# Performance work log

Measured on AMD Instinct MI355X. Metric: run time of the kernel, lower is better.

Reference implementation:

```python
import jax, jax.numpy as jnp
import numpy as np

B, S, D, A = 64, 2048, 512, 512


def setup_inputs() -> dict:
    key = jax.random.key(0)
    ks = jax.random.split(key, 6)
    return {
        "input": jax.random.normal(ks[0], (B, D), dtype=jnp.float32),
        "context": jax.random.normal(ks[1], (B, S, D), dtype=jnp.float32),
        "Wh": jax.random.uniform(ks[2], (D, A), dtype=jnp.float32, minval=-0.1, maxval=0.1),
        "Ws": jax.random.uniform(ks[3], (D, A), dtype=jnp.float32, minval=-0.1, maxval=0.1),
        "b_attn": jax.random.uniform(ks[4], (A,), dtype=jnp.float32, minval=-0.1, maxval=0.1),
        "va": jax.random.uniform(ks[5], (A,), dtype=jnp.float32, minval=-0.1, maxval=0.1),
    }


def reference(input, context, Wh, Ws, b_attn, va):
    # _concat score: tanh(ht@Wh + context@Ws + b) @ va  -> [B, S]
    ht_proj = input @ Wh                      # [B, A]
    ctx_proj = jnp.einsum("bsd,da->bsa", context, Ws)  # [B, S, A]
    concat = jnp.tanh(ht_proj[:, None, :] + ctx_proj + b_attn)  # [B, S, A]
    attn = jnp.einsum("bsa,a->bs", concat, va)  # [B, S]
    # padding mask: positions whose mean feature is exactly 0
    context_mask = jnp.mean(context, axis=-1) == 0  # [B, S]
    attn = jnp.where(context_mask, -jnp.inf, attn)
    attn_dist = jax.nn.softmax(attn, axis=1)  # [B, S]
    attn_context = jnp.einsum("bsd,bs->bd", context, attn_dist)  # [B, D]
    return attn_context, attn_dist
```

## Files before the change

### kernel.cpp

```cpp
#include <hip/hip_runtime.h>
#include <hip/hip_bf16.h>
#include <math.h>

#define B_ 64
#define S_ 2048
#define D_ 512
#define A_ 512

typedef __attribute__((ext_vector_type(8))) short short8;
typedef __attribute__((ext_vector_type(4))) short short4b;
typedef __attribute__((ext_vector_type(4))) float f32x4;

__device__ __forceinline__ short bf16b(float f) {
    __hip_bfloat16 h = __float2bfloat16(f);
    union { __hip_bfloat16 h; short s; } u; u.h = h;
    return u.s;
}

__device__ __forceinline__ float tanh_fast(float x) {
    float e = __expf(2.0f * x);
    return 1.0f - 2.0f / (e + 1.0f);
}

__device__ __forceinline__ void llds16(const void* g, void* l) {
    __builtin_amdgcn_global_load_lds(
        (const __attribute__((address_space(1))) unsigned int*)g,
        (__attribute__((address_space(3))) unsigned int*)l, 16, 0, 0);
}

__global__ __launch_bounds__(256) void k_htw(const float* __restrict__ input,
                                             const float* __restrict__ Wh,
                                             const float* __restrict__ b_attn,
                                             float* __restrict__ htWb) {
    __shared__ float xin[512];
    const int b = blockIdx.x, t = threadIdx.x;
    xin[t] = input[b * D_ + t];
    xin[t + 256] = input[b * D_ + t + 256];
    __syncthreads();
    float a0 = 0.f, a1 = 0.f;
#pragma unroll 8
    for (int d = 0; d < D_; ++d) {
        const float xv = xin[d];
        a0 += xv * Wh[d * A_ + t];
        a1 += xv * Wh[d * A_ + t + 256];
    }
    htWb[b * A_ + t] = a0 + b_attn[t];
    htWb[b * A_ + t + 256] = a1 + b_attn[t + 256];
}

__global__ __launch_bounds__(256) void k_wst(const float* __restrict__ Ws,
                                             short* __restrict__ WsT) {
    const int bx = blockIdx.x & 7, by = blockIdx.x >> 3;
    const int r0 = by * 64, c0 = bx * 64;
    __shared__ short tile[64][72];
    const int t = threadIdx.x;
    const int row = t >> 4, col4 = (t & 15) * 4;
#pragma unroll
    for (int i = 0; i < 4; ++i) {
        const float4 v = *(const float4*)&Ws[(r0 + row + i * 16) * A_ + c0 + col4];
        tile[col4 + 0][row + i * 16] = bf16b(v.x);
        tile[col4 + 1][row + i * 16] = bf16b(v.y);
        tile[col4 + 2][row + i * 16] = bf16b(v.z);
        tile[col4 + 3][row + i * 16] = bf16b(v.w);
    }
    __syncthreads();
#pragma unroll
    for (int i = 0; i < 4; ++i) {
        const int arow = row + i * 16;
        short4b o;
        o.x = tile[arow][col4 + 0];
        o.y = tile[arow][col4 + 1];
        o.z = tile[arow][col4 + 2];
        o.w = tile[arow][col4 + 3];
        *(short4b*)&WsT[(c0 + arow) * D_ + r0 + col4] = o;
    }
}

__global__ __launch_bounds__(512, 4)
void k_score(const float* __restrict__ ctx, const short* __restrict__ WsT,
             const float* __restrict__ htWb, const float* __restrict__ va,
             float* __restrict__ scores) {
    __shared__ __align__(16) short Ab[2][64 * 32];
    __shared__ __align__(16) short Bb[2][512 * 32];
    __shared__ float hv_s[512];
    __shared__ float va_s[512];
    __shared__ float scores_s[64];
    __shared__ float rowsum_s[64];

    const int tid = threadIdx.x;
    const int w = tid >> 6, lane = tid & 63;
    const int wm = w >> 2, wn = w & 3;
    const int tile = blockIdx.x;
    const int b = tile >> 5;
    const int s0 = (tile & 31) * 64;
    const long rowbase = (long)b * S_ + s0;

    hv_s[tid] = htWb[b * A_ + tid];
    va_s[tid] = va[tid];
    if (tid < 64) scores_s[tid] = 0.f;

    const int arow = tid >> 3, kq = tid & 7;
    const float* aSrc = ctx + (rowbase + arow) * D_ + kq * 4;
    float rowsum_acc = 0.f;

    f32x4 acc[2][8];
#pragma unroll
    for (int i = 0; i < 2; ++i)
#pragma unroll
        for (int j = 0; j < 8; ++j)
#pragma unroll
            for (int e = 0; e < 4; ++e) acc[i][j][e] = 0.f;

#define STAGE_B(buf, kt)                                                      \
    {                                                                         \
        _Pragma("unroll") for (int j = 0; j < 4; ++j) {                       \
            const int a = (w * 4 + j) * 16 + (lane >> 2);                     \
            const int c = lane & 3;                                           \
            const int csw = c ^ ((a >> 1) & 3);                               \
            llds16(WsT + a * D_ + (kt) * 32 + csw * 8,                        \
                   (void*)&Bb[buf][(w * 4 + j) * 512]);                       \
        }                                                                     \
    }

#define STAGE_A_WRITE(buf, v)                                                 \
    {                                                                         \
        rowsum_acc += (v).x + (v).y + (v).z + (v).w;                          \
        short4b o;                                                            \
        o.x = bf16b((v).x); o.y = bf16b((v).y);                               \
        o.z = bf16b((v).z); o.w = bf16b((v).w);                               \
        const int cw = kq >> 1, sub = kq & 1;                                 \
        const int csw = cw ^ ((arow >> 1) & 3);                               \
        *(short4b*)((char*)&Ab[buf][0] + arow * 64 + csw * 16 + sub * 8) = o; \
    }

    STAGE_B(0, 0);
    {
        const float4 v = *(const float4*)(aSrc);
        STAGE_A_WRITE(0, v);
    }
    __syncthreads();

    for (int kt = 0; kt < 16; ++kt) {
        const int cur = kt & 1;
        float4 nv;
        if (kt < 15) {
            nv = *(const float4*)(aSrc + (kt + 1) * 32);
            STAGE_B(cur ^ 1, kt + 1);
        }
        {
            short8 af[2];
#pragma unroll
            for (int mf = 0; mf < 2; ++mf) {
                const int r = wm * 32 + mf * 16 + (lane & 15);
                const int c = lane >> 4;
                const int csw = c ^ ((r >> 1) & 3);
                af[mf] = *(const short8*)((const char*)&Ab[cur][0] + r * 64 + csw * 16);
            }
#pragma unroll
            for (int nf = 0; nf < 8; ++nf) {
                const int a = wn * 128 + nf * 16 + (lane & 15);
                const int c = lane >> 4;
                const int csw = c ^ ((a >> 1) & 3);
                const short8 bf =
                    *(const short8*)((const char*)&Bb[cur][0] + a * 64 + csw * 16);
                acc[0][nf] = __builtin_amdgcn_mfma_f32_16x16x32_bf16(af[0], bf, acc[0][nf], 0, 0, 0);
                acc[1][nf] = __builtin_amdgcn_mfma_f32_16x16x32_bf16(af[1], bf, acc[1][nf], 0, 0, 0);
            }
        }
        if (kt < 15) STAGE_A_WRITE(cur ^ 1, nv);
        __syncthreads();
    }

    rowsum_acc += __shfl_xor(rowsum_acc, 1);
    rowsum_acc += __shfl_xor(rowsum_acc, 2);
    rowsum_acc += __shfl_xor(rowsum_acc, 4);
    if ((tid & 7) == 0) rowsum_s[arow] = rowsum_acc;

    float hv[8], vv[8];
#pragma unroll
    for (int nf = 0; nf < 8; ++nf) {
        const int col = wn * 128 + nf * 16 + (lane & 15);
        hv[nf] = hv_s[col];
        vv[nf] = va_s[col];
    }
#pragma unroll
    for (int mf = 0; mf < 2; ++mf) {
#pragma unroll
        for (int r = 0; r < 4; ++r) {
            float p = 0.f;
#pragma unroll
            for (int nf = 0; nf < 8; ++nf)
                p += vv[nf] * tanh_fast(hv[nf] + acc[mf][nf][r]);
            p += __shfl_xor(p, 1);
            p += __shfl_xor(p, 2);
            p += __shfl_xor(p, 4);
            p += __shfl_xor(p, 8);
            if ((lane & 15) == 0) {
                const int row = wm * 32 + mf * 16 + (lane >> 4) * 4 + r;
                atomicAdd(&scores_s[row], p);
            }
        }
    }
    __syncthreads();

    if (tid < 64) {
        float sc = scores_s[tid];
        if (rowsum_s[tid] == 0.0f) sc = -__builtin_inff();
        scores[rowbase + tid] = sc;
    }
}

__global__ __launch_bounds__(256) void k_softmax(float* __restrict__ dist) {
    const int b = blockIdx.x, t = threadIdx.x;
    float* p = dist + b * S_;
    float v[8];
    float m = -__builtin_inff();
#pragma unroll
    for (int i = 0; i < 8; ++i) {
        v[i] = p[t + i * 256];
        m = fmaxf(m, v[i]);
    }
#pragma unroll
    for (int mask = 1; mask < 64; mask <<= 1) m = fmaxf(m, __shfl_xor(m, mask));
    __shared__ float redm[4], reds[4];
    if ((t & 63) == 0) redm[t >> 6] = m;
    __syncthreads();
    m = fmaxf(fmaxf(redm[0], redm[1]), fmaxf(redm[2], redm[3]));
    float sum = 0.f;
#pragma unroll
    for (int i = 0; i < 8; ++i) {
        v[i] = __expf(v[i] - m);
        sum += v[i];
    }
#pragma unroll
    for (int mask = 1; mask < 64; mask <<= 1) sum += __shfl_xor(sum, mask);
    if ((t & 63) == 0) reds[t >> 6] = sum;
    __syncthreads();
    sum = reds[0] + reds[1] + reds[2] + reds[3];
    const float inv = 1.0f / sum;
#pragma unroll
    for (int i = 0; i < 8; ++i) p[t + i * 256] = v[i] * inv;
}

__global__ __launch_bounds__(256) void k_wsum(const float* __restrict__ ctx,
                                              const float* __restrict__ dist,
                                              float* __restrict__ partial) {
    const int ch = blockIdx.x, b = blockIdx.y;
    const int t = threadIdx.x;
    __shared__ float ps[128];
    if (t < 128) ps[t] = dist[b * S_ + ch * 128 + t];
    __syncthreads();
    const float* cbase = ctx + ((long)b * S_ + ch * 128) * D_;
    float ax = 0.f, ay = 0.f;
#pragma unroll 4
    for (int r = 0; r < 128; ++r) {
        const float2 cv = *(const float2*)&cbase[r * D_ + t * 2];
        ax += ps[r] * cv.x;
        ay += ps[r] * cv.y;
    }
    float2 o; o.x = ax; o.y = ay;
    *(float2*)&partial[((b * 16 + ch) * D_) + t * 2] = o;
}

__global__ __launch_bounds__(256) void k_reduce(const float* __restrict__ partial,
                                                float* __restrict__ out) {
    const int b = blockIdx.x, t = threadIdx.x;
    float ax = 0.f, ay = 0.f;
#pragma unroll
    for (int j = 0; j < 16; ++j) {
        const float2 v = *(const float2*)&partial[((b * 16 + j) * D_) + t * 2];
        ax += v.x;
        ay += v.y;
    }
    float2 o; o.x = ax; o.y = ay;
    *(float2*)&out[b * D_ + t * 2] = o;
}

extern "C" void kernel_launch(void* const* d_in, const int* in_sizes, int n_in,
                              void* d_out, int out_size, void* d_ws, size_t ws_size,
                              hipStream_t stream) {
    (void)in_sizes; (void)n_in; (void)out_size; (void)ws_size;
    const float* input  = (const float*)d_in[0];
    const float* ctx    = (const float*)d_in[1];
    const float* Wh     = (const float*)d_in[2];
    const float* Ws     = (const float*)d_in[3];
    const float* b_attn = (const float*)d_in[4];
    const float* va     = (const float*)d_in[5];

    float* out = (float*)d_out;
    float* attn_ctx  = out;
    float* attn_dist = out + B_ * D_;

    char* ws = (char*)d_ws;
    float* htWb    = (float*)ws;
    short* WsT     = (short*)(ws + 131072);
    float* partial = (float*)(ws + 131072 + 524288);

    k_htw<<<64, 256, 0, stream>>>(input, Wh, b_attn, htWb);
    k_wst<<<64, 256, 0, stream>>>(Ws, WsT);
    k_score<<<2048, 512, 0, stream>>>(ctx, WsT, htWb, va, attn_dist);
    k_softmax<<<64, 256, 0, stream>>>(attn_dist);
    k_wsum<<<dim3(16, 64), 256, 0, stream>>>(ctx, attn_dist, partial);
    k_reduce<<<64, 256, 0, stream>>>(partial, attn_ctx);
}
```

Before: 507.6 us.

## Double score-kernel M tile to 128 rows and widen wsum loads to float4

```diff
diff --git a/kernel.cpp b/kernel.cpp
--- a/kernel.cpp
+++ b/kernel.cpp
@@ -76,36 +76,36 @@
     }
 }
 
-__global__ __launch_bounds__(512, 4)
-void k_score(const float* __restrict__ ctx, const short* __restrict__ WsT,
-             const float* __restrict__ htWb, const float* __restrict__ va,
-             float* __restrict__ scores) {
-    __shared__ __align__(16) short Ab[2][64 * 32];
+__global__ __launch_bounds__(512, 2)
+void k_score2(const float* __restrict__ ctx, const short* __restrict__ WsT,
+              const float* __restrict__ htWb, const float* __restrict__ va,
+              float* __restrict__ scores) {
+    __shared__ __align__(16) short Ab[2][128 * 32];
     __shared__ __align__(16) short Bb[2][512 * 32];
     __shared__ float hv_s[512];
     __shared__ float va_s[512];
-    __shared__ float scores_s[64];
-    __shared__ float rowsum_s[64];
+    __shared__ float scores_s[128];
+    __shared__ float rowsum_s[128];
 
     const int tid = threadIdx.x;
     const int w = tid >> 6, lane = tid & 63;
     const int wm = w >> 2, wn = w & 3;
-    const int tile = blockIdx.x;
-    const int b = tile >> 5;
-    const int s0 = (tile & 31) * 64;
+    const int blk = blockIdx.x;
+    const int b = blk >> 4;
+    const int s0 = (blk & 15) * 128;
     const long rowbase = (long)b * S_ + s0;
 
     hv_s[tid] = htWb[b * A_ + tid];
     va_s[tid] = va[tid];
-    if (tid < 64) scores_s[tid] = 0.f;
-
-    const int arow = tid >> 3, kq = tid & 7;
-    const float* aSrc = ctx + (rowbase + arow) * D_ + kq * 4;
+    if (tid < 128) scores_s[tid] = 0.f;
+
+    const int arow = tid >> 2, aq = tid & 2 * 2 - 1;
+    const float* aSrc = ctx + (rowbase + arow) * (long)D_;
     float rowsum_acc = 0.f;
 
-    f32x4 acc[2][8];
-#pragma unroll
-    for (int i = 0; i < 2; ++i)
+    f32x4 acc[4][8];
+#pragma unroll
+    for (int i = 0; i < 4; ++i)
 #pragma unroll
         for (int j = 0; j < 8; ++j)
 #pragma unroll
@@ -122,36 +122,42 @@
         }                                                                     \
     }
 
-#define STAGE_A_WRITE(buf, v)                                                 \
+#define STAGE_A_WRITE(buf, v0, v1)                                            \
     {                                                                         \
-        rowsum_acc += (v).x + (v).y + (v).z + (v).w;                          \
-        short4b o;                                                            \
-        o.x = bf16b((v).x); o.y = bf16b((v).y);                               \
-        o.z = bf16b((v).z); o.w = bf16b((v).w);                               \
-        const int cw = kq >> 1, sub = kq & 1;                                 \
-        const int csw = cw ^ ((arow >> 1) & 3);                               \
-        *(short4b*)((char*)&Ab[buf][0] + arow * 64 + csw * 16 + sub * 8) = o; \
+        rowsum_acc += (v0).x + (v0).y + (v0).z + (v0).w;                      \
+        rowsum_acc += (v1).x + (v1).y + (v1).z + (v1).w;                      \
+        short4b o0, o1;                                                       \
+        o0.x = bf16b((v0).x); o0.y = bf16b((v0).y);                           \
+        o0.z = bf16b((v0).z); o0.w = bf16b((v0).w);                           \
+        o1.x = bf16b((v1).x); o1.y = bf16b((v1).y);                           \
+        o1.z = bf16b((v1).z); o1.w = bf16b((v1).w);                           \
+        const int sw = (arow >> 1) & 3;                                       \
+        const int c0 = (aq >> 1), c1 = 2 + (aq >> 1), sub = aq & 1;           \
+        *(short4b*)((char*)&Ab[buf][0] + arow * 64 + ((c0 ^ sw) * 16) + sub * 8) = o0; \
+        *(short4b*)((char*)&Ab[buf][0] + arow * 64 + ((c1 ^ sw) * 16) + sub * 8) = o1; \
     }
 
     STAGE_B(0, 0);
     {
-        const float4 v = *(const float4*)(aSrc);
-        STAGE_A_WRITE(0, v);
+        const float4 v0 = *(const float4*)(aSrc + aq * 4);
+        const float4 v1 = *(const float4*)(aSrc + aq * 4 + 16);
+        STAGE_A_WRITE(0, v0, v1);
     }
     __syncthreads();
 
     for (int kt = 0; kt < 16; ++kt) {
         const int cur = kt & 1;
-        float4 nv;
+        float4 nv0, nv1;
         if (kt < 15) {
-            nv = *(const float4*)(aSrc + (kt + 1) * 32);
             STAGE_B(cur ^ 1, kt + 1);
+            nv0 = *(const float4*)(aSrc + (kt + 1) * 32 + aq * 4);
+            nv1 = *(const float4*)(aSrc + (kt + 1) * 32 + aq * 4 + 16);
         }
         {
-            short8 af[2];
-#pragma unroll
-            for (int mf = 0; mf < 2; ++mf) {
-                const int r = wm * 32 + mf * 16 + (lane & 15);
+            short8 af[4];
+#pragma unroll
+            for (int mf = 0; mf < 4; ++mf) {
+                const int r = wm * 64 + mf * 16 + (lane & 15);
                 const int c = lane >> 4;
                 const int csw = c ^ ((r >> 1) & 3);
                 af[mf] = *(const short8*)((const char*)&Ab[cur][0] + r * 64 + csw * 16);
@@ -163,18 +169,19 @@
                 const int csw = c ^ ((a >> 1) & 3);
                 const short8 bf =
                     *(const short8*)((const char*)&Bb[cur][0] + a * 64 + csw * 16);
-                acc[0][nf] = __builtin_amdgcn_mfma_f32_16x16x32_bf16(af[0], bf, acc[0][nf], 0, 0, 0);
-                acc[1][nf] = __builtin_amdgcn_mfma_f32_16x16x32_bf16(af[1], bf, acc[1][nf], 0, 0, 0);
+#pragma unroll
+                for (int mf = 0; mf < 4; ++mf)
+                    acc[mf][nf] = __builtin_amdgcn_mfma_f32_16x16x32_bf16(
+                        af[mf], bf, acc[mf][nf], 0, 0, 0);
             }
         }
-        if (kt < 15) STAGE_A_WRITE(cur ^ 1, nv);
+        if (kt < 15) STAGE_A_WRITE(cur ^ 1, nv0, nv1);
         __syncthreads();
     }
 
     rowsum_acc += __shfl_xor(rowsum_acc, 1);
     rowsum_acc += __shfl_xor(rowsum_acc, 2);
-    rowsum_acc += __shfl_xor(rowsum_acc, 4);
-    if ((tid & 7) == 0) rowsum_s[arow] = rowsum_acc;
+    if ((tid & 3) == 0) rowsum_s[arow] = rowsum_acc;
 
     float hv[8], vv[8];
 #pragma unroll
@@ -184,26 +191,26 @@
         vv[nf] = va_s[col];
     }
 #pragma unroll
-    for (int mf = 0; mf < 2; ++mf) {
-#pragma unroll
-        for (int r = 0; r < 4; ++r) {
+    for (int mf = 0; mf < 4; ++mf) {
+#pragma unroll
+        for (int e = 0; e < 4; ++e) {
             float p = 0.f;
 #pragma unroll
             for (int nf = 0; nf < 8; ++nf)
-                p += vv[nf] * tanh_fast(hv[nf] + acc[mf][nf][r]);
+                p += vv[nf] * tanh_fast(hv[nf] + acc[mf][nf][e]);
             p += __shfl_xor(p, 1);
             p += __shfl_xor(p, 2);
             p += __shfl_xor(p, 4);
             p += __shfl_xor(p, 8);
             if ((lane & 15) == 0) {
-                const int row = wm * 32 + mf * 16 + (lane >> 4) * 4 + r;
+                const int row = wm * 64 + mf * 16 + (lane >> 4) * 4 + e;
                 atomicAdd(&scores_s[row], p);
             }
         }
     }
     __syncthreads();
 
-    if (tid < 64) {
+    if (tid < 128) {
         float sc = scores_s[tid];
         if (rowsum_s[tid] == 0.0f) sc = -__builtin_inff();
         scores[rowbase + tid] = sc;
@@ -242,38 +249,40 @@
     for (int i = 0; i < 8; ++i) p[t + i * 256] = v[i] * inv;
 }
 
-__global__ __launch_bounds__(256) void k_wsum(const float* __restrict__ ctx,
+__global__ __launch_bounds__(128) void k_wsum(const float* __restrict__ ctx,
                                               const float* __restrict__ dist,
                                               float* __restrict__ partial) {
     const int ch = blockIdx.x, b = blockIdx.y;
     const int t = threadIdx.x;
     __shared__ float ps[128];
-    if (t < 128) ps[t] = dist[b * S_ + ch * 128 + t];
+    ps[t] = dist[b * S_ + ch * 128 + t];
     __syncthreads();
     const float* cbase = ctx + ((long)b * S_ + ch * 128) * D_;
-    float ax = 0.f, ay = 0.f;
+    float ax = 0.f, ay = 0.f, az = 0.f, aw = 0.f;
 #pragma unroll 4
     for (int r = 0; r < 128; ++r) {
-        const float2 cv = *(const float2*)&cbase[r * D_ + t * 2];
-        ax += ps[r] * cv.x;
-        ay += ps[r] * cv.y;
-    }
-    float2 o; o.x = ax; o.y = ay;
-    *(float2*)&partial[((b * 16 + ch) * D_) + t * 2] = o;
-}
-
-__global__ __launch_bounds__(256) void k_reduce(const float* __restrict__ partial,
+        const float4 cv = *(const float4*)&cbase[r * D_ + t * 4];
+        const float pw = ps[r];
+        ax += pw * cv.x;
+        ay += pw * cv.y;
+        az += pw * cv.z;
+        aw += pw * cv.w;
+    }
+    float4 o; o.x = ax; o.y = ay; o.z = az; o.w = aw;
+    *(float4*)&partial[((b * 16 + ch) * D_) + t * 4] = o;
+}
+
+__global__ __launch_bounds__(128) void k_reduce(const float* __restrict__ partial,
                                                 float* __restrict__ out) {
     const int b = blockIdx.x, t = threadIdx.x;
-    float ax = 0.f, ay = 0.f;
+    float ax = 0.f, ay = 0.f, az = 0.f, aw = 0.f;
 #pragma unroll
     for (int j = 0; j < 16; ++j) {
-        const float2 v = *(const float2*)&partial[((b * 16 + j) * D_) + t * 2];
-        ax += v.x;
-        ay += v.y;
-    }
-    float2 o; o.x = ax; o.y = ay;
-    *(float2*)&out[b * D_ + t * 2] = o;
+        const float4 v = *(const float4*)&partial[((b * 16 + j) * D_) + t * 4];
+        ax += v.x; ay += v.y; az += v.z; aw += v.w;
+    }
+    float4 o; o.x = ax; o.y = ay; o.z = az; o.w = aw;
+    *(float4*)&out[b * D_ + t * 4] = o;
 }
 
 extern "C" void kernel_launch(void* const* d_in, const int* in_sizes, int n_in,
@@ -298,8 +307,8 @@
 
     k_htw<<<64, 256, 0, stream>>>(input, Wh, b_attn, htWb);
     k_wst<<<64, 256, 0, stream>>>(Ws, WsT);
-    k_score<<<2048, 512, 0, stream>>>(ctx, WsT, htWb, va, attn_dist);
+    k_score2<<<1024, 512, 0, stream>>>(ctx, WsT, htWb, va, attn_dist);
     k_softmax<<<64, 256, 0, stream>>>(attn_dist);
-    k_wsum<<<dim3(16, 64), 256, 0, stream>>>(ctx, attn_dist, partial);
-    k_reduce<<<64, 256, 0, stream>>>(partial, attn_ctx);
-}
+    k_wsum<<<dim3(16, 64), 128, 0, stream>>>(ctx, attn_dist, partial);
+    k_reduce<<<64, 128, 0, stream>>>(partial, attn_ctx);
+}
```

Result: slower. 519.5 us (+2.3%).
